# Kernel optimization log

Measured on AMD Instinct MI355X. Metric: run time of the kernel, lower is better.

Reference implementation:

```python
import jax, jax.numpy as jnp
import numpy as np
from jax import lax

NUM_FILTERS = 180
DN = ('NCHW', 'OIHW', 'NCHW')


def _gabor_kernel(freq, theta, sigma_x, sigma_y, n_stds=3):
    # real part of skimage.filters.gabor_kernel
    ct, st = np.cos(theta), np.sin(theta)
    x0 = int(np.ceil(max(abs(n_stds * sigma_x * ct), abs(n_stds * sigma_y * st), 1)))
    y0 = int(np.ceil(max(abs(n_stds * sigma_y * ct), abs(n_stds * sigma_x * st), 1)))
    y, x = np.mgrid[-y0:y0 + 1, -x0:x0 + 1]
    rotx = x * ct + y * st
    roty = -x * st + y * ct
    g = np.exp(-0.5 * (rotx ** 2 / sigma_x ** 2 + roty ** 2 / sigma_y ** 2))
    g /= 2.0 * np.pi * sigma_x * sigma_y
    return g * np.cos(2.0 * np.pi * freq * rotx)  # Re{exp(1j*2*pi*f*rotx)}


def _make_weights(sigma_x, sigma_y, freq, num_filters):
    kernels = [
        _gabor_kernel(freq, theta=np.pi - th, sigma_x=sigma_x, sigma_y=sigma_y)
        for th in np.linspace(0, np.pi * (num_filters - 1) / num_filters, num_filters)
    ]
    s = max(max(k.shape) for k in kernels)  # 17 for defaults
    kernels = np.stack([
        np.pad(k, [[(s - k.shape[0]) // 2], [(s - k.shape[1]) // 2]]) for k in kernels
    ])
    return kernels.astype(np.float32)


def _gauss1d(sigma, truncate=4.0):
    # matches scipy.ndimage gaussian kernel (skimage default truncate=4.0)
    r = int(truncate * sigma + 0.5)
    xs = np.arange(-r, r + 1, dtype=np.float64)
    k = np.exp(-0.5 * (xs / sigma) ** 2)
    return (k / k.sum()).astype(np.float32), r


def _gaussian_blur(img, sigma):
    # separable blur with edge-replicate ('nearest') padding, img: [B,1,H,W]
    k, r = _gauss1d(sigma)
    kh = jnp.asarray(k).reshape(1, 1, -1, 1)
    kw = jnp.asarray(k).reshape(1, 1, 1, -1)
    p = jnp.pad(img, ((0, 0), (0, 0), (r, r), (0, 0)), mode='edge')
    img = lax.conv_general_dilated(p, kh, (1, 1), 'VALID', dimension_numbers=DN)
    p = jnp.pad(img, ((0, 0), (0, 0), (0, 0), (r, r)), mode='edge')
    return lax.conv_general_dilated(p, kw, (1, 1), 'VALID', dimension_numbers=DN)


def setup_inputs() -> dict:
    key = jax.random.key(0)
    x = jax.random.uniform(key, (2, 3, 512, 512), dtype=jnp.float32)
    weights = jnp.asarray(_make_weights(1.8, 2.4, 0.23, NUM_FILTERS))[:, None, :, :]  # [180,1,17,17]
    bins = jnp.asarray(
        np.linspace(0, np.pi * (NUM_FILTERS - 1) / NUM_FILTERS, NUM_FILTERS), jnp.float32
    ).reshape(1, -1, 1, 1)
    return {'x': x, 'weights': weights, 'bins': bins}


def reference(x, weights, bins):
    # rgb -> gray, [B,1,H,W]
    gray = (0.2989 * x[:, 0] + 0.587 * x[:, 1] + 0.114 * x[:, 2])[:, None]
    # difference of gaussians (skimage, low=0.4, high=10.0)
    filtered = _gaussian_blur(gray, 0.4) - _gaussian_blur(gray, 10.0)
    kh, kw = weights.shape[2], weights.shape[3]
    response = lax.conv_general_dilated(
        filtered, weights, (1, 1), ((kh // 2, kh // 2), (kw // 2, kw // 2)),
        dimension_numbers=DN)  # [B,180,H,W]
    response = jnp.abs(response)
    idx = jnp.argmax(response, axis=1)[:, None]  # [B,1,H,W]
    orientation_map = idx.astype(jnp.float32) / NUM_FILTERS * 255.0
    orientation_map_rad = orientation_map / NUM_FILTERS * jnp.pi
    d0 = jnp.abs(orientation_map_rad - bins)
    dists = jnp.minimum(d0, jnp.minimum(jnp.abs(orientation_map_rad - bins - jnp.pi),
                                        jnp.abs(orientation_map_rad - bins + jnp.pi)))
    F_orients_norm = response / jnp.sum(response, axis=1, keepdims=True)
    confidence_map = jnp.sum(dists ** 2 * F_orients_norm, axis=1)  # [B,H,W]
    return orientation_map, confidence_map
```

## Files before the change

kernel.cpp:

```cpp
#include <hip/hip_runtime.h>
#include <math.h>
#include <stdint.h>

#define H 512
#define W 512
#define NPIX (H * W)
#define NB 2
#define NF 180
#define KS 17
#define WSCALE 1024.0f

#define RAW_U32 1440
#define BCH_U32 3072

typedef _Float16 half8 __attribute__((ext_vector_type(8)));
typedef float floatx16 __attribute__((ext_vector_type(16)));
typedef uint32_t u32x4 __attribute__((ext_vector_type(4)));

union FragU { u32x4 u; half8 h; };

__global__ void k_taps(float* __restrict__ taps) {
  if (threadIdx.x == 0 && blockIdx.x == 0) {
    {
      double k[5], s = 0.0;
      for (int i = 0; i < 5; i++) { double xv = (double)(i - 2) / 0.4; k[i] = exp(-0.5 * xv * xv); s += k[i]; }
      for (int i = 0; i < 5; i++) taps[i] = (float)(k[i] / s);
    }
    {
      double k[81], s = 0.0;
      for (int i = 0; i < 81; i++) { double xv = (double)(i - 40) / 10.0; k[i] = exp(-0.5 * xv * xv); s += k[i]; }
      for (int i = 0; i < 81; i++) taps[8 + i] = (float)(k[i] / s);
    }
  }
}

__global__ void k_repackB(const float* __restrict__ w, uint32_t* __restrict__ Bf) {
  int tid = blockIdx.x * 256 + threadIdx.x;
  if (tid >= 19 * 6 * 64 * 4) return;
  int q = tid & 3;
  int lane = (tid >> 2) & 63;
  int ct = tid >> 8;
  int t = ct % 6, c = ct / 6;
  int n = t * 32 + (lane & 31);
  int hf = lane >> 5;
  uint32_t hv = 0, lv = 0;
  for (int s = 0; s < 2; s++) {
    int j = 2 * q + s;
    int k = hf * 8 + j;
    float val = 0.f;
    if (n < NF) {
      if (c < 17)       val = w[n * 289 + c * 17 + k];
      else if (c == 17) val = w[n * 289 + k * 17 + 16];
      else if (k == 0)  val = w[n * 289 + 16 * 17 + 16];
    }
    val *= WSCALE;
    _Float16 hh = (_Float16)val;
    _Float16 ll = (_Float16)(val - (float)hh);
    hv |= (uint32_t)__builtin_bit_cast(uint16_t, hh) << (16 * s);
    lv |= (uint32_t)__builtin_bit_cast(uint16_t, ll) << (16 * s);
  }
  int base = c * 3072;
  int off = t * 256 + lane * 4 + q;
  Bf[base + off] = hv;
  Bf[base + 1536 + off] = lv;
}

__global__ void k_gray(const float* __restrict__ x, float* __restrict__ gray) {
  int i = blockIdx.x * blockDim.x + threadIdx.x;
  if (i >= NB * NPIX) return;
  int b = i / NPIX, r = i % NPIX;
  const float* xb = x + (size_t)b * 3 * NPIX;
  gray[i] = 0.2989f * xb[r] + 0.587f * xb[NPIX + r] + 0.114f * xb[2 * NPIX + r];
}

__global__ void k_vblur2(const float* __restrict__ in, float* __restrict__ outA,
                         float* __restrict__ outB, const float* __restrict__ taps) {
  int i = blockIdx.x * blockDim.x + threadIdx.x;
  if (i >= NB * NPIX) return;
  int b = i / NPIX, r = i % NPIX;
  int y = r / W, xx = r % W;
  const float* img = in + (size_t)b * NPIX;
  float a = 0.f;
#pragma unroll
  for (int j = -2; j <= 2; j++) {
    int yy = y + j; yy = yy < 0 ? 0 : (yy > H - 1 ? H - 1 : yy);
    a = fmaf(taps[j + 2], img[yy * W + xx], a);
  }
  float c = 0.f;
  for (int j = -40; j <= 40; j++) {
    int yy = y + j; yy = yy < 0 ? 0 : (yy > H - 1 ? H - 1 : yy);
    c = fmaf(taps[8 + j + 40], img[yy * W + xx], c);
  }
  outA[i] = a;
  outB[i] = c;
}

__global__ void k_hblur_dog(const float* __restrict__ inA, const float* __restrict__ inB,
                            uint32_t* __restrict__ dogp, const float* __restrict__ taps) {
  int i = blockIdx.x * blockDim.x + threadIdx.x;
  if (i >= NB * NPIX) return;
  int b = i / NPIX, r = i % NPIX;
  int y = r / W, xx = r % W;
  const float* ra = inA + (size_t)b * NPIX + (size_t)y * W;
  const float* rb = inB + (size_t)b * NPIX + (size_t)y * W;
  float a = 0.f;
#pragma unroll
  for (int j = -2; j <= 2; j++) {
    int xc = xx + j; xc = xc < 0 ? 0 : (xc > W - 1 ? W - 1 : xc);
    a = fmaf(taps[j + 2], ra[xc], a);
  }
  float c = 0.f;
  for (int j = -40; j <= 40; j++) {
    int xc = xx + j; xc = xc < 0 ? 0 : (xc > W - 1 ? W - 1 : xc);
    c = fmaf(taps[8 + j + 40], rb[xc], c);
  }
  float d = a - c;
  _Float16 hh = (_Float16)d;
  _Float16 ll = (_Float16)(d - (float)hh);
  dogp[i] = ((uint32_t)__builtin_bit_cast(uint16_t, ll) << 16) |
            (uint32_t)__builtin_bit_cast(uint16_t, hh);
}

__launch_bounds__(256, 2)
__global__ void k_conv(const uint32_t* __restrict__ dogp,
                       const uint32_t* __restrict__ Bf,
                       const float* __restrict__ bins,
                       float* __restrict__ out) {
  __shared__ uint32_t pool[RAW_U32];

  const int b  = blockIdx.z;
  const int y0 = blockIdx.y * 2;
  const int x0 = blockIdx.x * 64;
  const int tid = threadIdx.x;
  const int lane = tid & 63;
  const int w  = __builtin_amdgcn_readfirstlane(tid >> 6);
  const int fg  = w & 1;
  const int ch  = w >> 1;
  const int nl = lane & 31;
  const int half = lane >> 5;

  const uint32_t* dgb = dogp + (size_t)b * NPIX;
  for (int i = tid; i < 18 * 80; i += 256) {
    int ry = i / 80, rx = i % 80;
    int gy = y0 + ry - 8, gx = x0 + rx - 8;
    uint32_t v = 0;
    if (gy >= 0 && gy < H && gx >= 0 && gx < W) v = dgb[gy * W + gx];
    pool[i] = v;
  }
  __syncthreads();

  floatx16 acc[2][3];
#pragma unroll
  for (int d = 0; d < 2; d++)
#pragma unroll
    for (int t = 0; t < 3; t++)
#pragma unroll
      for (int q = 0; q < 16; q++) acc[d][t][q] = 0.f;

  const int abase = ch * 32 + nl + half * 8;

  auto buildRow = [&](int tr, FragU& fh, FragU& fl) {
    const uint32_t* rp = &pool[tr * 80 + abase];
    uint32_t d[8];
#pragma unroll
    for (int j = 0; j < 8; j++) d[j] = rp[j];
#pragma unroll
    for (int q = 0; q < 4; q++) {
      fh.u[q] = __builtin_amdgcn_perm(d[2 * q + 1], d[2 * q], 0x05040100u);
      fl.u[q] = __builtin_amdgcn_perm(d[2 * q + 1], d[2 * q], 0x07060302u);
    }
  };
  auto buildStrip = [&](int c, int rb, FragU& fh, FragU& fl) {
    int kyb = (c - 17) * 16 + half * 8;
    uint32_t d[8];
#pragma unroll
    for (int j = 0; j < 8; j++) {
      int ky = kyb + j; if (ky > 16) ky = 16;
      d[j] = pool[(rb + ky) * 80 + ch * 32 + nl + 16];
    }
#pragma unroll
    for (int q = 0; q < 4; q++) {
      fh.u[q] = __builtin_amdgcn_perm(d[2 * q + 1], d[2 * q], 0x05040100u);
      fl.u[q] = __builtin_amdgcn_perm(d[2 * q + 1], d[2 * q], 0x07060302u);
    }
  };
  auto mfma18 = [&](FragU* wh, FragU* wl,
                    FragU& d0h, FragU& d0l, FragU& d1h, FragU& d1l) {
#pragma unroll
    for (int t = 0; t < 3; t++) {
      acc[0][t] = __builtin_amdgcn_mfma_f32_32x32x16_f16(wh[t].h, d0h.h, acc[0][t], 0, 0, 0);
      acc[1][t] = __builtin_amdgcn_mfma_f32_32x32x16_f16(wh[t].h, d1h.h, acc[1][t], 0, 0, 0);
    }
#pragma unroll
    for (int t = 0; t < 3; t++) {
      acc[0][t] = __builtin_amdgcn_mfma_f32_32x32x16_f16(wh[t].h, d0l.h, acc[0][t], 0, 0, 0);
      acc[1][t] = __builtin_amdgcn_mfma_f32_32x32x16_f16(wh[t].h, d1l.h, acc[1][t], 0, 0, 0);
    }
#pragma unroll
    for (int t = 0; t < 3; t++) {
      acc[0][t] = __builtin_amdgcn_mfma_f32_32x32x16_f16(wl[t].h, d0h.h, acc[0][t], 0, 0, 0);
      acc[1][t] = __builtin_amdgcn_mfma_f32_32x32x16_f16(wl[t].h, d1h.h, acc[1][t], 0, 0, 0);
    }
  };

  const uint32_t* wbh = Bf + (size_t)(3 * fg) * 256 + (size_t)lane * 4;
  const uint32_t* wbl = wbh + 1536;

  FragU wch[3], wcl[3], wnh[3], wnl2[3];
#pragma unroll
  for (int t = 0; t < 3; t++) {
    wch[t].u = *(const u32x4*)(wbh + t * 256);
    wcl[t].u = *(const u32x4*)(wbl + t * 256);
  }

  FragU a0h, a0l, a1h, a1l;
  buildRow(0, a0h, a0l);

  for (int c = 0; c < 17; c++) {
    const uint32_t* nbh = wbh + (size_t)(c + 1) * BCH_U32;
    const uint32_t* nbl = wbl + (size_t)(c + 1) * BCH_U32;
#pragma unroll
    for (int t = 0; t < 3; t++) {
      wnh[t].u  = *(const u32x4*)(nbh + t * 256);
      wnl2[t].u = *(const u32x4*)(nbl + t * 256);
    }
    buildRow(c + 1, a1h, a1l);
    mfma18(wch, wcl, a0h, a0l, a1h, a1l);
    a0h = a1h; a0l = a1l;
#pragma unroll
    for (int t = 0; t < 3; t++) { wch[t] = wnh[t]; wcl[t] = wnl2[t]; }
  }
  {
    const uint32_t* nbh = wbh + (size_t)18 * BCH_U32;
    const uint32_t* nbl = wbl + (size_t)18 * BCH_U32;
#pragma unroll
    for (int t = 0; t < 3; t++) {
      wnh[t].u  = *(const u32x4*)(nbh + t * 256);
      wnl2[t].u = *(const u32x4*)(nbl + t * 256);
    }
    FragU s0h, s0l, s1h, s1l;
    buildStrip(17, 0, s0h, s0l);
    buildStrip(17, 1, s1h, s1l);
    mfma18(wch, wcl, s0h, s0l, s1h, s1l);
#pragma unroll
    for (int t = 0; t < 3; t++) { wch[t] = wnh[t]; wcl[t] = wnl2[t]; }
  }
  {
    FragU s0h, s0l, s1h, s1l;
    buildStrip(18, 0, s0h, s0l);
    buildStrip(18, 1, s1h, s1l);
    mfma18(wch, wcl, s0h, s0l, s1h, s1l);
  }
  __syncthreads();

  float* pm = (float*)&pool[0];
  int*   pn = (int*)&pool[256];
  float* pS = (float*)&pool[512];
  float* pc = (float*)&pool[768];
  int*   fn = (int*)&pool[1024];
  float* fS = (float*)&pool[1152];

  const float PI_F = 3.14159265358979323846f;
  const float INV_PI = 0.31830988618379067154f;
  const double STEPD = 3.14159265358979323846 * 179.0 / 180.0 / 179.0;
  const float stepf = (float)STEPD;
  const float hbase = (4.0f * (float)half) * stepf;
  const int colp = ch * 32 + nl;

#pragma unroll
  for (int d = 0; d < 2; d++) {
    float m = -1.f; int n = 0; float S0 = 0.f, S1 = 0.f;
#pragma unroll
    for (int t = 0; t < 3; t++) {
#pragma unroll
      for (int q = 0; q < 16; q++) {
        float v = fabsf(acc[d][t][q]);
        if (q & 1) S1 += v; else S0 += v;
        int nf = 32 * (3 * fg + t) + (q & 3) + 8 * (q >> 2) + 4 * half;
        if (v > m) { m = v; n = nf; }
      }
    }
    float S = S0 + S1;
    float mo = __shfl_xor(m, 32);
    int   no = __shfl_xor(n, 32);
    float So = __shfl_xor(S, 32);
    bool take = (mo > m) || (mo == m && no < n);
    if (take) { m = mo; n = no; }
    S += So;
    if (half == 0) {
      int o = (d * 2 + fg) * 64 + colp;
      pm[o] = m; pn[o] = n; pS[o] = S;
    }
  }
  __syncthreads();

  if (fg == 0) {
#pragma unroll
    for (int d = 0; d < 2; d++) {
      int o0 = (d * 2 + 0) * 64 + colp;
      int o1 = (d * 2 + 1) * 64 + colp;
      float m0 = pm[o0], m1 = pm[o1];
      int n = (m1 > m0) ? pn[o1] : pn[o0];
      float S = pS[o0] + pS[o1];
      float om = (float)n / 180.0f * 255.0f;
      if (half == 0) {
        fn[d * 64 + colp] = n; fS[d * 64 + colp] = S;
        out[(size_t)b * NPIX + (size_t)(y0 + d) * W + x0 + colp] = om;
      }
    }
  }
  __syncthreads();

#pragma unroll
  for (int d = 0; d < 2; d++) {
    int nwin = fn[d * 64 + colp];
    float om = (float)nwin / 180.0f * 255.0f;
    float rad = om / 180.0f * PI_F;
    float ddc = rad - hbase;
    float C0 = 0.f, C1 = 0.f;
#pragma unroll
    for (int t = 0; t < 3; t++) {
#pragma unroll
      for (int q = 0; q < 16; q++) {
        const float K = (float)((double)(32 * (3 * fg + t) + (q & 3) + 8 * (q >> 2)) * STEPD);
        float dd = ddc - K;
        float r = rintf(dd * INV_PI);
        float dist = fmaf(-PI_F, r, dd);
        float w2 = dist * dist;
        if (q & 1) C1 = fmaf(w2, fabsf(acc[d][t][q]), C1);
        else       C0 = fmaf(w2, fabsf(acc[d][t][q]), C0);
      }
    }
    float C = C0 + C1;
    C += __shfl_xor(C, 32);
    if (half == 0) pc[(d * 2 + fg) * 64 + colp] = C;
  }
  __syncthreads();

  if (fg == 0) {
#pragma unroll
    for (int d = 0; d < 2; d++) {
      float C = pc[(d * 2 + 0) * 64 + colp] + pc[(d * 2 + 1) * 64 + colp];
      if (half == 0) {
        out[(size_t)NB * NPIX + (size_t)b * NPIX + (size_t)(y0 + d) * W + x0 + colp]
            = C / fS[d * 64 + colp];
      }
    }
  }
}

extern "C" void kernel_launch(void* const* d_in, const int* in_sizes, int n_in,
                              void* d_out, int out_size, void* d_ws, size_t ws_size,
                              hipStream_t stream) {
  const float* x = (const float*)d_in[0];
  const float* wts = (const float*)d_in[1];
  const float* bins = (const float*)d_in[2];
  float* out = (float*)d_out;

  float* ws = (float*)d_ws;
  float* gray = ws;
  float* tmpA = ws + (size_t)NB * NPIX;
  float* tmpB = tmpA + (size_t)NB * NPIX;
  uint32_t* dogp = (uint32_t*)(tmpB + (size_t)NB * NPIX);
  float* taps = (float*)(dogp + (size_t)NB * NPIX);
  uint32_t* Bf = (uint32_t*)(taps + 128);

  k_taps<<<1, 64, 0, stream>>>(taps);
  k_repackB<<<114, 256, 0, stream>>>(wts, Bf);

  int n = NB * NPIX;
  int blk = 256, grd = (n + blk - 1) / blk;
  k_gray<<<grd, blk, 0, stream>>>(x, gray);
  k_vblur2<<<grd, blk, 0, stream>>>(gray, tmpA, tmpB, taps);
  k_hblur_dog<<<grd, blk, 0, stream>>>(tmpA, tmpB, dogp, taps);

  dim3 g(W / 64, H / 2, NB);
  k_conv<<<g, 256, 0, stream>>>(dogp, Bf, bins, out);
}
```

Before: 191.5 us.

## Process one output row per block in Gabor conv to cut register pressure

The MFMA conv kernel now computes a single output row per block instead of two, halving the accumulator set (3 instead of 6 floatx16) and the LDS tile, and raising the launch-bounds occupancy hint from 2 to 3 blocks per CU. The grid doubles in the y dimension. The aim is higher occupancy and less register spilling. In exchange, each weight fragment loaded from global memory is reused for only one row, so weight traffic and halo loads per output pixel roughly double.

```diff
diff --git a/kernel.cpp b/kernel.cpp
--- a/kernel.cpp
+++ b/kernel.cpp
@@ -10,7 +10,7 @@
 #define KS 17
 #define WSCALE 1024.0f
 
-#define RAW_U32 1440
+#define RAW_U32 1360
 #define BCH_U32 3072
 
 typedef _Float16 half8 __attribute__((ext_vector_type(8)));
@@ -121,7 +121,7 @@
             (uint32_t)__builtin_bit_cast(uint16_t, hh);
 }
 
-__launch_bounds__(256, 2)
+__launch_bounds__(256, 3)
 __global__ void k_conv(const uint32_t* __restrict__ dogp,
                        const uint32_t* __restrict__ Bf,
                        const float* __restrict__ bins,
@@ -129,7 +129,7 @@
   __shared__ uint32_t pool[RAW_U32];
 
   const int b  = blockIdx.z;
-  const int y0 = blockIdx.y * 2;
+  const int y0 = blockIdx.y;
   const int x0 = blockIdx.x * 64;
   const int tid = threadIdx.x;
   const int lane = tid & 63;
@@ -140,7 +140,7 @@
   const int half = lane >> 5;
 
   const uint32_t* dgb = dogp + (size_t)b * NPIX;
-  for (int i = tid; i < 18 * 80; i += 256) {
+  for (int i = tid; i < 17 * 80; i += 256) {
     int ry = i / 80, rx = i % 80;
     int gy = y0 + ry - 8, gx = x0 + rx - 8;
     uint32_t v = 0;
@@ -149,13 +149,11 @@
   }
   __syncthreads();
 
-  floatx16 acc[2][3];
-#pragma unroll
-  for (int d = 0; d < 2; d++)
-#pragma unroll
-    for (int t = 0; t < 3; t++)
-#pragma unroll
-      for (int q = 0; q < 16; q++) acc[d][t][q] = 0.f;
+  floatx16 acc[3];
+#pragma unroll
+  for (int t = 0; t < 3; t++)
+#pragma unroll
+    for (int q = 0; q < 16; q++) acc[t][q] = 0.f;
 
   const int abase = ch * 32 + nl + half * 8;
 
@@ -170,13 +168,13 @@
       fl.u[q] = __builtin_amdgcn_perm(d[2 * q + 1], d[2 * q], 0x07060302u);
     }
   };
-  auto buildStrip = [&](int c, int rb, FragU& fh, FragU& fl) {
+  auto buildStrip = [&](int c, FragU& fh, FragU& fl) {
     int kyb = (c - 17) * 16 + half * 8;
     uint32_t d[8];
 #pragma unroll
     for (int j = 0; j < 8; j++) {
       int ky = kyb + j; if (ky > 16) ky = 16;
-      d[j] = pool[(rb + ky) * 80 + ch * 32 + nl + 16];
+      d[j] = pool[ky * 80 + ch * 32 + nl + 16];
     }
 #pragma unroll
     for (int q = 0; q < 4; q++) {
@@ -184,23 +182,16 @@
       fl.u[q] = __builtin_amdgcn_perm(d[2 * q + 1], d[2 * q], 0x07060302u);
     }
   };
-  auto mfma18 = [&](FragU* wh, FragU* wl,
-                    FragU& d0h, FragU& d0l, FragU& d1h, FragU& d1l) {
-#pragma unroll
-    for (int t = 0; t < 3; t++) {
-      acc[0][t] = __builtin_amdgcn_mfma_f32_32x32x16_f16(wh[t].h, d0h.h, acc[0][t], 0, 0, 0);
-      acc[1][t] = __builtin_amdgcn_mfma_f32_32x32x16_f16(wh[t].h, d1h.h, acc[1][t], 0, 0, 0);
-    }
-#pragma unroll
-    for (int t = 0; t < 3; t++) {
-      acc[0][t] = __builtin_amdgcn_mfma_f32_32x32x16_f16(wh[t].h, d0l.h, acc[0][t], 0, 0, 0);
-      acc[1][t] = __builtin_amdgcn_mfma_f32_32x32x16_f16(wh[t].h, d1l.h, acc[1][t], 0, 0, 0);
-    }
-#pragma unroll
-    for (int t = 0; t < 3; t++) {
-      acc[0][t] = __builtin_amdgcn_mfma_f32_32x32x16_f16(wl[t].h, d0h.h, acc[0][t], 0, 0, 0);
-      acc[1][t] = __builtin_amdgcn_mfma_f32_32x32x16_f16(wl[t].h, d1h.h, acc[1][t], 0, 0, 0);
-    }
+  auto mfma9 = [&](FragU* wh, FragU* wl, FragU& dh, FragU& dl) {
+#pragma unroll
+    for (int t = 0; t < 3; t++)
+      acc[t] = __builtin_amdgcn_mfma_f32_32x32x16_f16(wh[t].h, dh.h, acc[t], 0, 0, 0);
+#pragma unroll
+    for (int t = 0; t < 3; t++)
+      acc[t] = __builtin_amdgcn_mfma_f32_32x32x16_f16(wh[t].h, dl.h, acc[t], 0, 0, 0);
+#pragma unroll
+    for (int t = 0; t < 3; t++)
+      acc[t] = __builtin_amdgcn_mfma_f32_32x32x16_f16(wl[t].h, dh.h, acc[t], 0, 0, 0);
   };
 
   const uint32_t* wbh = Bf + (size_t)(3 * fg) * 256 + (size_t)lane * 4;
@@ -213,9 +204,9 @@
     wcl[t].u = *(const u32x4*)(wbl + t * 256);
   }
 
-  FragU a0h, a0l, a1h, a1l;
-  buildRow(0, a0h, a0l);
-
+  FragU ah, al;
+
+#pragma unroll
   for (int c = 0; c < 17; c++) {
     const uint32_t* nbh = wbh + (size_t)(c + 1) * BCH_U32;
     const uint32_t* nbl = wbl + (size_t)(c + 1) * BCH_U32;
@@ -224,9 +215,8 @@
       wnh[t].u  = *(const u32x4*)(nbh + t * 256);
       wnl2[t].u = *(const u32x4*)(nbl + t * 256);
     }
-    buildRow(c + 1, a1h, a1l);
-    mfma18(wch, wcl, a0h, a0l, a1h, a1l);
-    a0h = a1h; a0l = a1l;
+    buildRow(c, ah, al);
+    mfma9(wch, wcl, ah, al);
 #pragma unroll
     for (int t = 0; t < 3; t++) { wch[t] = wnh[t]; wcl[t] = wnl2[t]; }
   }
@@ -238,27 +228,25 @@
       wnh[t].u  = *(const u32x4*)(nbh + t * 256);
       wnl2[t].u = *(const u32x4*)(nbl + t * 256);
     }
-    FragU s0h, s0l, s1h, s1l;
-    buildStrip(17, 0, s0h, s0l);
-    buildStrip(17, 1, s1h, s1l);
-    mfma18(wch, wcl, s0h, s0l, s1h, s1l);
+    FragU sh, sl;
+    buildStrip(17, sh, sl);
+    mfma9(wch, wcl, sh, sl);
 #pragma unroll
     for (int t = 0; t < 3; t++) { wch[t] = wnh[t]; wcl[t] = wnl2[t]; }
   }
   {
-    FragU s0h, s0l, s1h, s1l;
-    buildStrip(18, 0, s0h, s0l);
-    buildStrip(18, 1, s1h, s1l);
-    mfma18(wch, wcl, s0h, s0l, s1h, s1l);
+    FragU sh, sl;
+    buildStrip(18, sh, sl);
+    mfma9(wch, wcl, sh, sl);
   }
   __syncthreads();
 
   float* pm = (float*)&pool[0];
-  int*   pn = (int*)&pool[256];
-  float* pS = (float*)&pool[512];
-  float* pc = (float*)&pool[768];
-  int*   fn = (int*)&pool[1024];
-  float* fS = (float*)&pool[1152];
+  int*   pn = (int*)&pool[128];
+  float* pS = (float*)&pool[256];
+  float* pc = (float*)&pool[384];
+  int*   fn = (int*)&pool[512];
+  float* fS = (float*)&pool[576];
 
   const float PI_F = 3.14159265358979323846f;
   const float INV_PI = 0.31830988618379067154f;
@@ -267,14 +255,13 @@
   const float hbase = (4.0f * (float)half) * stepf;
   const int colp = ch * 32 + nl;
 
-#pragma unroll
-  for (int d = 0; d < 2; d++) {
+  {
     float m = -1.f; int n = 0; float S0 = 0.f, S1 = 0.f;
 #pragma unroll
     for (int t = 0; t < 3; t++) {
 #pragma unroll
       for (int q = 0; q < 16; q++) {
-        float v = fabsf(acc[d][t][q]);
+        float v = fabsf(acc[t][q]);
         if (q & 1) S1 += v; else S0 += v;
         int nf = 32 * (3 * fg + t) + (q & 3) + 8 * (q >> 2) + 4 * half;
         if (v > m) { m = v; n = nf; }
@@ -288,32 +275,28 @@
     if (take) { m = mo; n = no; }
     S += So;
     if (half == 0) {
-      int o = (d * 2 + fg) * 64 + colp;
+      int o = fg * 64 + colp;
       pm[o] = m; pn[o] = n; pS[o] = S;
     }
   }
   __syncthreads();
 
   if (fg == 0) {
-#pragma unroll
-    for (int d = 0; d < 2; d++) {
-      int o0 = (d * 2 + 0) * 64 + colp;
-      int o1 = (d * 2 + 1) * 64 + colp;
-      float m0 = pm[o0], m1 = pm[o1];
-      int n = (m1 > m0) ? pn[o1] : pn[o0];
-      float S = pS[o0] + pS[o1];
-      float om = (float)n / 180.0f * 255.0f;
-      if (half == 0) {
-        fn[d * 64 + colp] = n; fS[d * 64 + colp] = S;
-        out[(size_t)b * NPIX + (size_t)(y0 + d) * W + x0 + colp] = om;
-      }
-    }
-  }
-  __syncthreads();
-
-#pragma unroll
-  for (int d = 0; d < 2; d++) {
-    int nwin = fn[d * 64 + colp];
+    int o0 = 0 * 64 + colp;
+    int o1 = 1 * 64 + colp;
+    float m0 = pm[o0], m1 = pm[o1];
+    int n = (m1 > m0) ? pn[o1] : pn[o0];
+    float S = pS[o0] + pS[o1];
+    float om = (float)n / 180.0f * 255.0f;
+    if (half == 0) {
+      fn[colp] = n; fS[colp] = S;
+      out[(size_t)b * NPIX + (size_t)y0 * W + x0 + colp] = om;
+    }
+  }
+  __syncthreads();
+
+  {
+    int nwin = fn[colp];
     float om = (float)nwin / 180.0f * 255.0f;
     float rad = om / 180.0f * PI_F;
     float ddc = rad - hbase;
@@ -327,24 +310,21 @@
         float r = rintf(dd * INV_PI);
         float dist = fmaf(-PI_F, r, dd);
         float w2 = dist * dist;
-        if (q & 1) C1 = fmaf(w2, fabsf(acc[d][t][q]), C1);
-        else       C0 = fmaf(w2, fabsf(acc[d][t][q]), C0);
+        if (q & 1) C1 = fmaf(w2, fabsf(acc[t][q]), C1);
+        else       C0 = fmaf(w2, fabsf(acc[t][q]), C0);
       }
     }
     float C = C0 + C1;
     C += __shfl_xor(C, 32);
-    if (half == 0) pc[(d * 2 + fg) * 64 + colp] = C;
+    if (half == 0) pc[fg * 64 + colp] = C;
   }
   __syncthreads();
 
   if (fg == 0) {
-#pragma unroll
-    for (int d = 0; d < 2; d++) {
-      float C = pc[(d * 2 + 0) * 64 + colp] + pc[(d * 2 + 1) * 64 + colp];
-      if (half == 0) {
-        out[(size_t)NB * NPIX + (size_t)b * NPIX + (size_t)(y0 + d) * W + x0 + colp]
-            = C / fS[d * 64 + colp];
-      }
+    float C = pc[0 * 64 + colp] + pc[1 * 64 + colp];
+    if (half == 0) {
+      out[(size_t)NB * NPIX + (size_t)b * NPIX + (size_t)y0 * W + x0 + colp]
+          = C / fS[colp];
     }
   }
 }
@@ -374,6 +354,6 @@
   k_vblur2<<<grd, blk, 0, stream>>>(gray, tmpA, tmpB, taps);
   k_hblur_dog<<<grd, blk, 0, stream>>>(tmpA, tmpB, dogp, taps);
 
-  dim3 g(W / 64, H / 2, NB);
+  dim3 g(W / 64, H, NB);
   k_conv<<<g, 256, 0, stream>>>(dogp, Bf, bins, out);
 }
```

Measured after the change: 227.6 us. 1.19x slower.
